# Optimization experiments

Hardware: AMD Instinct MI355X
Metric: run time of the kernel (lower is better)

Reference implementation:

```python
import jax, jax.numpy as jnp
import numpy as np

N_NODES = 50000
N_EDGES = 300000
N_GRAPHS = 2048
N_FEATS = 128
DIM_OUT = 32


def setup_inputs() -> dict:
    key = jax.random.key(0)
    ks = jax.random.split(key, 10)
    def glorot(k, shape):
        fan_in, fan_out = shape
        lim = (6.0 / (fan_in + fan_out)) ** 0.5
        return jax.random.uniform(k, shape, jnp.float32, -lim, lim)
    x = jax.random.normal(ks[0], (N_NODES, N_FEATS), jnp.float32)
    edge_index = jax.random.randint(ks[1], (2, N_EDGES), 0, N_NODES, jnp.int64)
    batch = jnp.sort(jax.random.randint(ks[2], (N_NODES,), 0, N_GRAPHS, jnp.int64))
    return {
        "x": x,
        "edge_index": edge_index,
        "batch": batch,
        "W1": glorot(ks[3], (N_FEATS, 256)), "b1": jnp.zeros((256,), jnp.float32),
        "W2": glorot(ks[4], (256, 256)),     "b2": jnp.zeros((256,), jnp.float32),
        "W3": glorot(ks[5], (256, 256)),     "b3": jnp.zeros((256,), jnp.float32),
        "Wf1": glorot(ks[6], (256, 128)),    "bf1": jnp.zeros((128,), jnp.float32),
        "Wf2": glorot(ks[7], (128, DIM_OUT)), "bf2": jnp.zeros((DIM_OUT,), jnp.float32),
    }


def _gcn_norm(edge_index, num_nodes):
    # PyG GCNConv default: add self-loops, symmetric D^-1/2 (A+I) D^-1/2 norm.
    loop = jnp.arange(num_nodes, dtype=edge_index.dtype)
    src = jnp.concatenate([edge_index[0], loop])
    dst = jnp.concatenate([edge_index[1], loop])
    deg = jax.ops.segment_sum(jnp.ones_like(dst, jnp.float32), dst, num_segments=num_nodes)
    dinv = jnp.where(deg > 0, deg ** -0.5, 0.0)
    norm = dinv[src] * dinv[dst]  # [E + N]
    return src, dst, norm


def _gcn_conv(x, src, dst, norm, W, b):
    h = x @ W                                # [N, C] transform first (efficient)
    msg = h[src] * norm[:, None]             # gather + scale, [E+N, C]
    agg = jax.ops.segment_sum(msg, dst, num_segments=x.shape[0])
    return agg + b


def reference(x, edge_index, batch, W1, b1, W2, b2, W3, b3, Wf1, bf1, Wf2, bf2):
    n = x.shape[0]
    src, dst, norm = _gcn_norm(edge_index, n)
    h = jax.nn.relu(_gcn_conv(x, src, dst, norm, W1, b1))
    h = jax.nn.relu(_gcn_conv(h, src, dst, norm, W2, b2))
    h = jax.nn.relu(_gcn_conv(h, src, dst, norm, W3, b3))
    # global_mean_pool over batch segment ids
    sums = jax.ops.segment_sum(h, batch, num_segments=N_GRAPHS)
    cnts = jax.ops.segment_sum(jnp.ones((n,), jnp.float32), batch, num_segments=N_GRAPHS)
    hg = sums / jnp.maximum(cnts, 1.0)[:, None]
    h = jax.nn.relu(hg @ Wf1 + bf1)
    return h @ Wf2 + bf2  # [N_GRAPHS, DIM_OUT]
```

## Files before the change

kernel.cpp:

```cpp
#include <hip/hip_runtime.h>
#include <hip/hip_bf16.h>

#define NNODES 50000
#define NEDGES 300000
#define NGRAPH 2048
#define NFEAT  128
#define NHID   256
#define DOUT   32
#define NROWS  50048

typedef __bf16 bf16x8 __attribute__((ext_vector_type(8)));
typedef float  f32x4  __attribute__((ext_vector_type(4)));
typedef unsigned short ushort8v __attribute__((ext_vector_type(8)));
typedef __attribute__((address_space(1))) const void* gas_ptr;
typedef __attribute__((address_space(3))) void* las_ptr;

__device__ __forceinline__ float bf2f(unsigned short u) {
    return __uint_as_float(((unsigned)u) << 16);
}
__device__ __forceinline__ unsigned short f2bf(float f) {
    unsigned u = __float_as_uint(f);
    unsigned r = u + 0x7FFFu + ((u >> 16) & 1u);
    return (unsigned short)(r >> 16);
}
__device__ __forceinline__ float sb2f(unsigned v, int k) {
    return (float)((signed char)(v >> (8 * k)));
}


__global__ __launch_bounds__(256) void prep_k(const float* __restrict__ x, unsigned short* __restrict__ x16,
                                              const float* __restrict__ W1, const float* __restrict__ W2,
                                              const float* __restrict__ W3, const float* __restrict__ Wf1,
                                              const float* __restrict__ Wf2,
                                              unsigned short* __restrict__ Wt1, unsigned short* __restrict__ Wt2,
                                              unsigned short* __restrict__ Wt3, unsigned short* __restrict__ Wf1t,
                                              unsigned short* __restrict__ Wf2t,
                                              int* __restrict__ cnt, int* __restrict__ fill,
                                              int4* __restrict__ adj8z, float4* __restrict__ hgz) {
    int idx = blockIdx.x * 256 + threadIdx.x;
    if (idx < 800000) {
        int i = idx * 8;
        float4 a = *(const float4*)&x[i];
        float4 b = *(const float4*)&x[i + 4];
        ushort8v o = { f2bf(a.x), f2bf(a.y), f2bf(a.z), f2bf(a.w),
                       f2bf(b.x), f2bf(b.y), f2bf(b.z), f2bf(b.w) };
        int row = idx >> 4, ch = idx & 15;
        ((ushort8v*)x16)[(size_t)(row << 4) | (ch ^ (row & 7))] = o;
        return;
    }
    int t = idx - 800000;
    if (t < 200704) {
        const float* W; unsigned short* Wt; int K, N, base; bool sw;
        if      (t <  32768) { W = W1;  Wt = Wt1;  K = 128; N = 256; base = 0;      sw = true; }
        else if (t <  98304) { W = W2;  Wt = Wt2;  K = 256; N = 256; base = 32768;  sw = true; }
        else if (t < 163840) { W = W3;  Wt = Wt3;  K = 256; N = 256; base = 98304;  sw = true; }
        else if (t < 196608) { W = Wf1; Wt = Wf1t; K = 256; N = 128; base = 163840; sw = false; }
        else                 { W = Wf2; Wt = Wf2t; K = 128; N = 32;  base = 196608; sw = false; }
        int i = t - base; int n = i / K, k = i - n * K;
        unsigned short v = f2bf(W[(size_t)k * N + n]);
        if (sw) Wt[(k >> 5) * 8192 + n * 32 + (k & 31)] = v;
        else    Wt[i] = v;
        return;
    }
    t -= 200704;
    if (t < NNODES) { cnt[t] = 0; fill[t] = 0; return; }
    t -= NNODES;
    if (t < 200000) { int4 z4 = {0, 0, 0, 0}; adj8z[t] = z4; return; }
    t -= 200000;
    if (t < 131072) { hgz[t] = make_float4(0.f, 0.f, 0.f, 0.f); }
}

__global__ __launch_bounds__(256) void edge_hist_k(const int* __restrict__ dst, int* cnt, int E) {
    int e = blockIdx.x * 256 + threadIdx.x;
    if (e < E) atomicAdd(&cnt[dst[e]], 1);
}

__global__ __launch_bounds__(1024) void scan_block_k(const int* __restrict__ cnt, int* __restrict__ rowp,
                                                     int* __restrict__ part, float* __restrict__ dinv,
                                                     int2* __restrict__ hdr, int n) {
    __shared__ int s[1024];
    int tid = threadIdx.x;
    int i = blockIdx.x * 1024 + tid;
    int v = (i < n) ? cnt[i] : 0;
    if (i < n) {
        float dv = rsqrtf((float)(v + 1));
        dinv[i] = dv;
        hdr[i] = make_int2(v, __float_as_int(dv * dv));
    }
    s[tid] = v;
    __syncthreads();
    for (int off = 1; off < 1024; off <<= 1) {
        int t = (tid >= off) ? s[tid - off] : 0;
        __syncthreads();
        s[tid] += t;
        __syncthreads();
    }
    if (i < n) rowp[i] = s[tid] - v;
    if (tid == 1023) part[blockIdx.x] = s[1023];
}

__global__ __launch_bounds__(256) void scatter_k(const int* __restrict__ src, const int* __restrict__ dst,
                                                 const int* __restrict__ rowp_pre, const int* __restrict__ part,
                                                 int* fill, const float* __restrict__ dinv,
                                                 int2* __restrict__ adj8, int2* __restrict__ adj,
                                                 int* __restrict__ rowp_fin,
                                                 const int* __restrict__ batch, int* __restrict__ gstart,
                                                 int E, int n, int nb) {
    __shared__ int s[64];
    int tid = threadIdx.x;
    if (tid < 64) s[tid] = (tid < nb) ? part[tid] : 0;
    __syncthreads();
    for (int off = 1; off < 64; off <<= 1) {
        int t = 0;
        if (tid < 64 && tid >= off) t = s[tid - off];
        __syncthreads();
        if (tid < 64) s[tid] += t;
        __syncthreads();
    }
    int gid = blockIdx.x * 256 + tid;
    if (gid <= n) {
        if (gid < n) {
            int ch = gid >> 10;
            int base = (ch == 0) ? 0 : s[ch - 1];
            rowp_fin[gid] = rowp_pre[gid] + base;
        } else {
            rowp_fin[n] = s[nb - 1];
        }
    }
    if (gid < n) {
        int b = batch[gid];
        int prev = (gid == 0) ? -1 : batch[gid - 1];
        for (int g = prev + 1; g <= b; ++g) gstart[g] = gid;
        if (gid == n - 1)
            for (int g = b + 1; g <= NGRAPH; ++g) gstart[g] = n;
    }
    if (gid < E) {
        int ss = src[gid], d = dst[gid];
        int f = atomicAdd(&fill[d], 1);
        int2 a; a.x = ss; a.y = __float_as_int(dinv[ss] * dinv[d]);
        if (f < 8) {
            adj8[d * 8 + f] = a;
        } else {
            int ch = d >> 10;
            int base = (ch == 0) ? 0 : s[ch - 1];
            adj[rowp_pre[d] + base + f] = a;
        }
    }
}

template<int CH>
__global__ __launch_bounds__(256) void agg_k(const unsigned short* __restrict__ T,
                                             const int4* __restrict__ adj8,
                                             const int2* __restrict__ hdr,
                                             const int* __restrict__ rowf,
                                             const int2* __restrict__ adj,
                                             unsigned short* __restrict__ z, int n) {
    int g  = threadIdx.x / CH;
    int li = threadIdx.x % CH;
    int node = blockIdx.x * (256 / CH) + g;
    if (node >= n) return;
    const ushort8v* tp = (const ushort8v*)T;
    int2 h = hdr[node];
    int deg = h.x;
    float sw = __int_as_float(h.y);
    ushort8v u = tp[(size_t)node * CH + (li ^ (node & 7))];
    int4 s4[4];
#pragma unroll
    for (int j = 0; j < 4; ++j) s4[j] = adj8[node * 4 + j];
    float ac[8];
#pragma unroll
    for (int k = 0; k < 8; ++k) ac[k] = bf2f(u[k]) * sw;
    int c[8]; float w[8];
#pragma unroll
    for (int j = 0; j < 4; ++j) {
        c[2 * j]     = s4[j].x; w[2 * j]     = __int_as_float(s4[j].y);
        c[2 * j + 1] = s4[j].z; w[2 * j + 1] = __int_as_float(s4[j].w);
    }
    ushort8v mm[8];
#pragma unroll
    for (int j = 0; j < 8; ++j) mm[j] = tp[(size_t)c[j] * CH + (li ^ (c[j] & 7))];
#pragma unroll
    for (int j = 0; j < 8; ++j)
#pragma unroll
        for (int k = 0; k < 8; ++k)
            ac[k] += bf2f(mm[j][k]) * w[j];
    if (deg > 8) {
        int e0 = rowf[node], e1 = e0 + deg;
        for (int e = e0 + 8; e < e1; e += 4) {
            int2 a2[4];
#pragma unroll
            for (int j = 0; j < 4; ++j) {
                int ee = e + j;
                a2[j] = (ee < e1) ? adj[ee] : make_int2(0, 0);
            }
            ushort8v m2[4];
#pragma unroll
            for (int j = 0; j < 4; ++j) m2[j] = tp[(size_t)a2[j].x * CH + (li ^ (a2[j].x & 7))];
#pragma unroll
            for (int j = 0; j < 4; ++j)
#pragma unroll
                for (int k = 0; k < 8; ++k)
                    ac[k] += bf2f(m2[j][k]) * __int_as_float(a2[j].y);
        }
    }
    ushort8v o;
#pragma unroll
    for (int k = 0; k < 8; ++k) o[k] = f2bf(ac[k]);
    ((ushort8v*)z)[(size_t)node * CH + (li ^ (node & 7))] = o;
}

__global__ __launch_bounds__(256) void agg_q_k(const unsigned char* __restrict__ Hq,
                                               const float* __restrict__ csc,
                                               const int4* __restrict__ adj8,
                                               const int2* __restrict__ hdr,
                                               const int* __restrict__ rowf,
                                               const int2* __restrict__ adj,
                                               unsigned short* __restrict__ z, int n) {
    int g  = threadIdx.x >> 4;
    int li = threadIdx.x & 15;
    int node = blockIdx.x * 16 + g;
    if (node >= n) return;
    const uint4* qp = (const uint4*)Hq;
    int2 h = hdr[node];
    int deg = h.x;
    float swgt = __int_as_float(h.y) * csc[node];
    uint4 u = qp[(size_t)node * 16 + li];
    int4 s4[4];
#pragma unroll
    for (int j = 0; j < 4; ++j) s4[j] = adj8[node * 4 + j];
    int c[8]; float w[8];
#pragma unroll
    for (int j = 0; j < 4; ++j) {
        c[2 * j]     = s4[j].x; w[2 * j]     = __int_as_float(s4[j].y);
        c[2 * j + 1] = s4[j].z; w[2 * j + 1] = __int_as_float(s4[j].w);
    }
    uint4 mm[8];
#pragma unroll
    for (int j = 0; j < 8; ++j) mm[j] = qp[(size_t)c[j] * 16 + li];
    float ws[8];
#pragma unroll
    for (int j = 0; j < 8; ++j) ws[j] = w[j] * csc[c[j]];
    float ac[16];
#pragma unroll
    for (int k = 0; k < 4; ++k) {
        ac[k]      = sb2f(u.x, k) * swgt;
        ac[k + 4]  = sb2f(u.y, k) * swgt;
        ac[k + 8]  = sb2f(u.z, k) * swgt;
        ac[k + 12] = sb2f(u.w, k) * swgt;
    }
#pragma unroll
    for (int j = 0; j < 8; ++j)
#pragma unroll
        for (int k = 0; k < 4; ++k) {
            ac[k]      += sb2f(mm[j].x, k) * ws[j];
            ac[k + 4]  += sb2f(mm[j].y, k) * ws[j];
            ac[k + 8]  += sb2f(mm[j].z, k) * ws[j];
            ac[k + 12] += sb2f(mm[j].w, k) * ws[j];
        }
    if (deg > 8) {
        int e0 = rowf[node], e1 = e0 + deg;
        for (int e = e0 + 8; e < e1; e += 4) {
            int2 a2[4];
#pragma unroll
            for (int j = 0; j < 4; ++j) {
                int ee = e + j;
                a2[j] = (ee < e1) ? adj[ee] : make_int2(0, 0);
            }
            uint4 m2[4]; float w2[4];
#pragma unroll
            for (int j = 0; j < 4; ++j) m2[j] = qp[(size_t)a2[j].x * 16 + li];
#pragma unroll
            for (int j = 0; j < 4; ++j) w2[j] = __int_as_float(a2[j].y) * csc[a2[j].x];
#pragma unroll
            for (int j = 0; j < 4; ++j)
#pragma unroll
                for (int k = 0; k < 4; ++k) {
                    ac[k]      += sb2f(m2[j].x, k) * w2[j];
                    ac[k + 4]  += sb2f(m2[j].y, k) * w2[j];
                    ac[k + 8]  += sb2f(m2[j].z, k) * w2[j];
                    ac[k + 12] += sb2f(m2[j].w, k) * w2[j];
                }
        }
    }
    ushort8v o0, o1;
#pragma unroll
    for (int k = 0; k < 8; ++k) { o0[k] = f2bf(ac[k]); o1[k] = f2bf(ac[k + 8]); }
    size_t base = (size_t)node * 32;
    ((ushort8v*)z)[base + ((2 * li)     ^ (node & 7))] = o0;
    ((ushort8v*)z)[base + ((2 * li + 1) ^ (node & 7))] = o1;
}

template<int K, int MODE>
__global__ __launch_bounds__(512, 2) void gemm_k(const unsigned short* __restrict__ A,
                                                 const unsigned short* __restrict__ Bsw,
                                                 const float* __restrict__ bias,
                                                 unsigned char* __restrict__ Cq,
                                                 float* __restrict__ csc,
                                                 float* __restrict__ HGacc,
                                                 const int* __restrict__ batch,
                                                 int M, int flags, int ntiles) {
    constexpr int CPR = K / 8;
    constexpr int LP  = (64 * CPR) / 512;
    __shared__ unsigned short At[64 * K];
    __shared__ unsigned short Et[64 * 264];
    __shared__ int sbatch[64];
    const int tid = threadIdx.x;
    const int lane = tid & 63;
    const int wave = tid >> 6;
    const int m = lane & 15, q = lane >> 4;
    const int wr = (wave >> 2) * 32;
    const int wc = (wave & 3) * 64;

    bf16x8 breg[K / 32][4];
#pragma unroll
    for (int kt = 0; kt < K / 32; ++kt)
#pragma unroll
        for (int j = 0; j < 4; ++j)
            breg[kt][j] = *(const bf16x8*)&Bsw[kt * 8192 + (wc + j * 16 + m) * 32 + q * 8];

    for (int t = blockIdx.x; t < ntiles; t += gridDim.x) {
        const size_t cbase = (size_t)t * 64 * CPR;
#pragma unroll
        for (int p = 0; p < LP; ++p) {
            int u = p * 512 + tid;
            __builtin_amdgcn_global_load_lds((gas_ptr)(A + (cbase + u) * 8),
                                             (las_ptr)&At[(p * 512 + wave * 64) * 8], 16, 0, 0);
        }
        __syncthreads();

        f32x4 acc[2][4] = {};
#pragma unroll
        for (int kt = 0; kt < K / 32; ++kt) {
            bf16x8 af[2];
#pragma unroll
            for (int i = 0; i < 2; ++i) {
                int lr = wr + i * 16 + m;
                af[i] = *(const bf16x8*)&At[(lr * CPR + ((kt * 4 + q) ^ (lr & 7))) * 8];
            }
#pragma unroll
            for (int i = 0; i < 2; ++i)
#pragma unroll
                for (int j = 0; j < 4; ++j)
                    acc[i][j] = __builtin_amdgcn_mfma_f32_16x16x32_bf16(af[i], breg[kt][j], acc[i][j], 0, 0, 0);
        }

#pragma unroll
        for (int i = 0; i < 2; ++i) {
#pragma unroll
            for (int j = 0; j < 4; ++j) {
                int c = wc + j * 16 + m;
                float bv = (flags & 2) ? bias[c] : 0.f;
#pragma unroll
                for (int r = 0; r < 4; ++r) {
                    float v = acc[i][j][r] + bv;
                    if (flags & 1) v = fmaxf(v, 0.f);
                    Et[(wr + i * 16 + q * 4 + r) * 264 + c] = f2bf(v);
                }
            }
        }
        if (MODE == 2 && tid < 64) {
            int rr = t * 64 + tid;
            sbatch[tid] = (rr < M) ? batch[rr] : -1;
        }
        __syncthreads();

        if (MODE == 1) {
            int row = tid >> 3, ch8 = tid & 7;
            int rr = t * 64 + row;
            ushort8v e[4];
#pragma unroll
            for (int k2 = 0; k2 < 4; ++k2)
                e[k2] = *(const ushort8v*)&Et[row * 264 + ch8 * 32 + k2 * 8];
            float mx = 0.f;
#pragma unroll
            for (int k2 = 0; k2 < 4; ++k2)
#pragma unroll
                for (int k = 0; k < 8; ++k) mx = fmaxf(mx, fabsf(bf2f(e[k2][k])));
            mx = fmaxf(mx, __shfl_xor(mx, 1, 64));
            mx = fmaxf(mx, __shfl_xor(mx, 2, 64));
            mx = fmaxf(mx, __shfl_xor(mx, 4, 64));
            float inv = (mx > 0.f) ? 127.f / mx : 0.f;
            unsigned pk[8];
#pragma unroll
            for (int w2 = 0; w2 < 8; ++w2) {
                unsigned p = 0;
#pragma unroll
                for (int b = 0; b < 4; ++b) {
                    int e8 = w2 * 4 + b;
                    float v = bf2f(e[e8 >> 3][e8 & 7]);
                    int qv = (int)rintf(v * inv);
                    p |= ((unsigned)(qv & 255)) << (8 * b);
                }
                pk[w2] = p;
            }
            if (rr < M) {
                uint4* dst = (uint4*)&Cq[(size_t)rr * 256 + ch8 * 32];
                dst[0] = make_uint4(pk[0], pk[1], pk[2], pk[3]);
                dst[1] = make_uint4(pk[4], pk[5], pk[6], pk[7]);
                if (ch8 == 0) csc[rr] = mx * (1.f / 127.f);
            }
        } else {
            int c = tid & 255, hh = tid >> 8;
            int gcur = sbatch[hh * 32];
            float acp = 0.f;
#pragma unroll 1
            for (int r = 0; r < 32; ++r) {
                int gb = sbatch[hh * 32 + r];
                if (gb != gcur) {
                    if (gcur >= 0) atomicAdd(&HGacc[(size_t)gcur * 256 + c], acp);
                    acp = 0.f; gcur = gb;
                }
                if (gb >= 0) acp += bf2f(Et[(hh * 32 + r) * 264 + c]);
            }
            if (gcur >= 0) atomicAdd(&HGacc[(size_t)gcur * 256 + c], acp);
        }
    }
}

__global__ __launch_bounds__(256) void mlp_head_k(const float* __restrict__ HGacc,
                                                  const int* __restrict__ gstart,
                                                  const unsigned short* __restrict__ Wf1t,
                                                  const unsigned short* __restrict__ Wf2t,
                                                  const float* __restrict__ bf1, const float* __restrict__ bf2,
                                                  float* __restrict__ out) {
    __shared__ unsigned short As1[128 * 32];
    __shared__ unsigned short Bs1[128 * 32];
    __shared__ unsigned short R[128 * 128];
    __shared__ unsigned short Bs2[32 * 128];
    __shared__ float invc[128];
    const int tid = threadIdx.x;
    const int lane = tid & 63, wave = tid >> 6;
    const int m = lane & 15, q = lane >> 4;
    const int rowBase = blockIdx.x * 128;
    const int wr = (wave >> 1) * 64;
    const int wc = (wave & 1) * 64;

#pragma unroll
    for (int c2 = 0; c2 < 2; ++c2) {
        const unsigned short* g = &Wf2t[(c2 * 256 + tid) * 8];
        __builtin_amdgcn_global_load_lds((gas_ptr)g, (las_ptr)&Bs2[(c2 * 256 + wave * 64) * 8], 16, 0, 0);
    }
    if (tid < 128) {
        int g0 = rowBase + tid;
        invc[tid] = 1.f / fmaxf((float)(gstart[g0 + 1] - gstart[g0]), 1.f);
    }
    __syncthreads();

    f32x4 acc[4][4] = {};
    for (int kt = 0; kt < 256; kt += 32) {
        {
            int row = tid >> 1, half = tid & 1;
            const float4* src = (const float4*)&HGacc[(size_t)(rowBase + row) * 256 + kt + half * 16];
            float4 f0 = src[0], f1 = src[1], f2 = src[2], f3 = src[3];
            float sc = invc[row];
            ushort8v p0 = { f2bf(f0.x * sc), f2bf(f0.y * sc), f2bf(f0.z * sc), f2bf(f0.w * sc),
                            f2bf(f1.x * sc), f2bf(f1.y * sc), f2bf(f1.z * sc), f2bf(f1.w * sc) };
            ushort8v p1 = { f2bf(f2.x * sc), f2bf(f2.y * sc), f2bf(f2.z * sc), f2bf(f2.w * sc),
                            f2bf(f3.x * sc), f2bf(f3.y * sc), f2bf(f3.z * sc), f2bf(f3.w * sc) };
            *(ushort8v*)&As1[row * 32 + half * 16] = p0;
            *(ushort8v*)&As1[row * 32 + half * 16 + 8] = p1;
        }
#pragma unroll
        for (int c2 = 0; c2 < 2; ++c2) {
            int u = c2 * 256 + tid;
            int row = u >> 2, kp = u & 3;
            const unsigned short* gb = &Wf1t[(size_t)row * 256 + kt + kp * 8];
            __builtin_amdgcn_global_load_lds((gas_ptr)gb, (las_ptr)&Bs1[(c2 * 256 + wave * 64) * 8], 16, 0, 0);
        }
        __syncthreads();
        bf16x8 af[4], bfr[4];
#pragma unroll
        for (int i = 0; i < 4; ++i) af[i] = *(const bf16x8*)&As1[(wr + i * 16 + m) * 32 + q * 8];
#pragma unroll
        for (int j = 0; j < 4; ++j) bfr[j] = *(const bf16x8*)&Bs1[(wc + j * 16 + m) * 32 + q * 8];
#pragma unroll
        for (int i = 0; i < 4; ++i)
#pragma unroll
            for (int j = 0; j < 4; ++j)
                acc[i][j] = __builtin_amdgcn_mfma_f32_16x16x32_bf16(af[i], bfr[j], acc[i][j], 0, 0, 0);
        __syncthreads();
    }
#pragma unroll
    for (int i = 0; i < 4; ++i)
#pragma unroll
        for (int j = 0; j < 4; ++j) {
            int c = wc + j * 16 + m;
            float bv = bf1[c];
#pragma unroll
            for (int r = 0; r < 4; ++r) {
                int rr = wr + i * 16 + q * 4 + r;
                R[rr * 128 + c] = f2bf(fmaxf(acc[i][j][r] + bv, 0.f));
            }
        }
    __syncthreads();

    const int wr2 = wave * 32;
    f32x4 acc2[2][2] = {};
#pragma unroll
    for (int s2 = 0; s2 < 4; ++s2) {
        bf16x8 af2[2], bf22[2];
#pragma unroll
        for (int i = 0; i < 2; ++i) af2[i] = *(const bf16x8*)&R[(wr2 + i * 16 + m) * 128 + s2 * 32 + q * 8];
#pragma unroll
        for (int ct = 0; ct < 2; ++ct) bf22[ct] = *(const bf16x8*)&Bs2[(ct * 16 + m) * 128 + s2 * 32 + q * 8];
#pragma unroll
        for (int i = 0; i < 2; ++i)
#pragma unroll
            for (int ct = 0; ct < 2; ++ct)
                acc2[i][ct] = __builtin_amdgcn_mfma_f32_16x16x32_bf16(af2[i], bf22[ct], acc2[i][ct], 0, 0, 0);
    }
#pragma unroll
    for (int i = 0; i < 2; ++i)
#pragma unroll
        for (int ct = 0; ct < 2; ++ct) {
            int c = ct * 16 + m;
            float bv = bf2[c];
#pragma unroll
            for (int r = 0; r < 4; ++r) {
                int rr = rowBase + wr2 + i * 16 + q * 4 + r;
                out[(size_t)rr * 32 + c] = acc2[i][ct][r] + bv;
            }
        }
}

extern "C" void kernel_launch(void* const* d_in, const int* in_sizes, int n_in,
                              void* d_out, int out_size, void* d_ws, size_t ws_size,
                              hipStream_t stream) {
    const float* x    = (const float*)d_in[0];
    const int*   ei   = (const int*)d_in[1];
    const int*   batch= (const int*)d_in[2];
    const float* W1   = (const float*)d_in[3];
    const float* b1   = (const float*)d_in[4];
    const float* W2   = (const float*)d_in[5];
    const float* b2   = (const float*)d_in[6];
    const float* W3   = (const float*)d_in[7];
    const float* b3   = (const float*)d_in[8];
    const float* Wf1  = (const float*)d_in[9];
    const float* bf1  = (const float*)d_in[10];
    const float* Wf2  = (const float*)d_in[11];
    const float* bf2  = (const float*)d_in[12];
    float* out = (float*)d_out;

    const int* e_src = ei;
    const int* e_dst = ei + NEDGES;

    char* ws = (char*)d_ws;
    size_t off = 0;
    auto alloc = [&](size_t bytes) -> void* {
        void* p = (void*)(ws + off);
        off += (bytes + 255) & ~(size_t)255;
        return p;
    };
    unsigned short* X16 = (unsigned short*)alloc((size_t)NROWS * NFEAT * 2);
    unsigned short* Za  = (unsigned short*)alloc((size_t)NROWS * NFEAT * 2);
    unsigned short* Zb  = (unsigned short*)alloc((size_t)NROWS * NHID * 2);
    unsigned char*  Hq  = (unsigned char*)alloc((size_t)NROWS * NHID);
    float*          csc = (float*)alloc((size_t)NROWS * 4);
    float*          HGacc = (float*)alloc((size_t)NGRAPH * NHID * 4);
    unsigned short* Wt1 = (unsigned short*)alloc((size_t)NHID * NFEAT * 2);
    unsigned short* Wt2 = (unsigned short*)alloc((size_t)NHID * NHID * 2);
    unsigned short* Wt3 = (unsigned short*)alloc((size_t)NHID * NHID * 2);
    unsigned short* Wf1t= (unsigned short*)alloc((size_t)NFEAT * NHID * 2);
    unsigned short* Wf2t= (unsigned short*)alloc((size_t)DOUT * NFEAT * 2);
    float* dinv = (float*)alloc((size_t)NNODES * 4);
    int*   cnt  = (int*)alloc((size_t)NNODES * 4);
    int*   fill = (int*)alloc((size_t)NNODES * 4);
    int*   rowp = (int*)alloc((size_t)(NNODES + 1) * 4);
    int*   rowf = (int*)alloc((size_t)(NNODES + 1) * 4);
    int2*  adj8 = (int2*)alloc((size_t)NNODES * 8 * 8);
    int2*  adj  = (int2*)alloc((size_t)NEDGES * 8);
    int2*  hdr  = (int2*)alloc((size_t)NNODES * 8);
    int*   part = (int*)alloc((size_t)64 * 4);
    int*   gstart = (int*)alloc((size_t)(NGRAPH + 1) * 4);
    (void)alloc(131072);

    const int nb = (NNODES + 1023) / 1024;

    hipLaunchKernelGGL(prep_k, dim3((1381776 + 255) / 256), dim3(256), 0, stream,
                       x, X16, W1, W2, W3, Wf1, Wf2, Wt1, Wt2, Wt3, Wf1t, Wf2t, cnt, fill,
                       (int4*)adj8, (float4*)HGacc);
    hipLaunchKernelGGL(edge_hist_k, dim3((NEDGES + 255) / 256), dim3(256), 0, stream, e_dst, cnt, NEDGES);
    hipLaunchKernelGGL(scan_block_k, dim3(nb), dim3(1024), 0, stream, cnt, rowp, part, dinv, hdr, NNODES);
    hipLaunchKernelGGL(scatter_k, dim3((NEDGES + 255) / 256), dim3(256), 0, stream,
                       e_src, e_dst, rowp, part, fill, dinv, adj8, adj, rowf, batch, gstart,
                       NEDGES, NNODES, nb);

    const int ntiles = NROWS / 64;
    hipLaunchKernelGGL((agg_k<16>), dim3((NNODES + 15) / 16), dim3(256), 0, stream,
                       X16, (const int4*)adj8, hdr, rowf, adj, Za, NNODES);
    hipLaunchKernelGGL((gemm_k<128, 1>), dim3(512), dim3(512), 0, stream,
                       Za, Wt1, b1, Hq, csc, (float*)nullptr, (const int*)nullptr, NNODES, 3, ntiles);
    hipLaunchKernelGGL(agg_q_k, dim3((NNODES + 15) / 16), dim3(256), 0, stream,
                       Hq, csc, (const int4*)adj8, hdr, rowf, adj, Zb, NNODES);
    hipLaunchKernelGGL((gemm_k<256, 1>), dim3(512), dim3(512), 0, stream,
                       Zb, Wt2, b2, Hq, csc, (float*)nullptr, (const int*)nullptr, NNODES, 3, ntiles);
    hipLaunchKernelGGL(agg_q_k, dim3((NNODES + 15) / 16), dim3(256), 0, stream,
                       Hq, csc, (const int4*)adj8, hdr, rowf, adj, Zb, NNODES);
    hipLaunchKernelGGL((gemm_k<256, 2>), dim3(512), dim3(512), 0, stream,
                       Zb, Wt3, b3, (unsigned char*)nullptr, (float*)nullptr, HGacc, batch, NNODES, 3, ntiles);

    hipLaunchKernelGGL(mlp_head_k, dim3(NGRAPH / 128), dim3(256), 0, stream,
                       HGacc, gstart, Wf1t, Wf2t, bf1, bf2, out);
}
```

Baseline: 275.6 us.

## Quantize input features to int8 and widen aggregation lanes per node

The input features are now quantized to int8 with a per-row scale in prep_k instead of converted to bf16, and a new agg_q1_k gathers these int8 rows for the first aggregation, halving the bytes gathered per neighbor. The layer 2/3 aggregation kernel is changed from 16 to 32 lanes per node with 8 bytes per lane, which halves the registers per thread and increases parallelism. The cost is lower precision on the raw inputs, plus an extra scale lookup per neighbor.

```diff
diff --git a/kernel.cpp b/kernel.cpp
--- a/kernel.cpp
+++ b/kernel.cpp
@@ -28,7 +28,8 @@
 }
 
 
-__global__ __launch_bounds__(256) void prep_k(const float* __restrict__ x, unsigned short* __restrict__ x16,
+__global__ __launch_bounds__(256) void prep_k(const float* __restrict__ x, unsigned char* __restrict__ Xq,
+                                              float* __restrict__ xsc,
                                               const float* __restrict__ W1, const float* __restrict__ W2,
                                               const float* __restrict__ W3, const float* __restrict__ Wf1,
                                               const float* __restrict__ Wf2,
@@ -39,13 +40,27 @@
                                               int4* __restrict__ adj8z, float4* __restrict__ hgz) {
     int idx = blockIdx.x * 256 + threadIdx.x;
     if (idx < 800000) {
-        int i = idx * 8;
-        float4 a = *(const float4*)&x[i];
-        float4 b = *(const float4*)&x[i + 4];
-        ushort8v o = { f2bf(a.x), f2bf(a.y), f2bf(a.z), f2bf(a.w),
-                       f2bf(b.x), f2bf(b.y), f2bf(b.z), f2bf(b.w) };
-        int row = idx >> 4, ch = idx & 15;
-        ((ushort8v*)x16)[(size_t)(row << 4) | (ch ^ (row & 7))] = o;
+        int row = idx >> 4, li = idx & 15;
+        const float4* xs = (const float4*)&x[(size_t)row * 128 + li * 8];
+        float4 a = xs[0], b = xs[1];
+        float m = fmaxf(fmaxf(fmaxf(fabsf(a.x), fabsf(a.y)), fmaxf(fabsf(a.z), fabsf(a.w))),
+                        fmaxf(fmaxf(fabsf(b.x), fabsf(b.y)), fmaxf(fabsf(b.z), fabsf(b.w))));
+        m = fmaxf(m, __shfl_xor(m, 1, 16));
+        m = fmaxf(m, __shfl_xor(m, 2, 16));
+        m = fmaxf(m, __shfl_xor(m, 4, 16));
+        m = fmaxf(m, __shfl_xor(m, 8, 16));
+        float inv = (m > 0.f) ? 127.f / m : 0.f;
+        float v[8] = {a.x, a.y, a.z, a.w, b.x, b.y, b.z, b.w};
+        unsigned w0 = 0, w1 = 0;
+#pragma unroll
+        for (int k = 0; k < 4; ++k) {
+            int q0 = (int)rintf(v[k] * inv);
+            int q1 = (int)rintf(v[k + 4] * inv);
+            w0 |= ((unsigned)(q0 & 255)) << (8 * k);
+            w1 |= ((unsigned)(q1 & 255)) << (8 * k);
+        }
+        ((uint2*)Xq)[(size_t)row * 16 + li] = make_uint2(w0, w1);
+        if (li == 0) xsc[row] = m * (1.f / 127.f);
         return;
     }
     int t = idx - 800000;
@@ -148,42 +163,50 @@
     }
 }
 
-template<int CH>
-__global__ __launch_bounds__(256) void agg_k(const unsigned short* __restrict__ T,
-                                             const int4* __restrict__ adj8,
-                                             const int2* __restrict__ hdr,
-                                             const int* __restrict__ rowf,
-                                             const int2* __restrict__ adj,
-                                             unsigned short* __restrict__ z, int n) {
-    int g  = threadIdx.x / CH;
-    int li = threadIdx.x % CH;
-    int node = blockIdx.x * (256 / CH) + g;
+__global__ __launch_bounds__(256) void agg_q1_k(const unsigned char* __restrict__ Xq,
+                                                const float* __restrict__ xsc,
+                                                const int4* __restrict__ adj8,
+                                                const int2* __restrict__ hdr,
+                                                const int* __restrict__ rowf,
+                                                const int2* __restrict__ adj,
+                                                unsigned short* __restrict__ z, int n) {
+    int g  = threadIdx.x >> 4;
+    int li = threadIdx.x & 15;
+    int node = blockIdx.x * 16 + g;
     if (node >= n) return;
-    const ushort8v* tp = (const ushort8v*)T;
+    const uint2* qp = (const uint2*)Xq;
     int2 h = hdr[node];
     int deg = h.x;
-    float sw = __int_as_float(h.y);
-    ushort8v u = tp[(size_t)node * CH + (li ^ (node & 7))];
+    float swgt = __int_as_float(h.y) * xsc[node];
+    uint2 u = qp[(size_t)node * 16 + li];
     int4 s4[4];
 #pragma unroll
     for (int j = 0; j < 4; ++j) s4[j] = adj8[node * 4 + j];
-    float ac[8];
-#pragma unroll
-    for (int k = 0; k < 8; ++k) ac[k] = bf2f(u[k]) * sw;
     int c[8]; float w[8];
 #pragma unroll
     for (int j = 0; j < 4; ++j) {
         c[2 * j]     = s4[j].x; w[2 * j]     = __int_as_float(s4[j].y);
         c[2 * j + 1] = s4[j].z; w[2 * j + 1] = __int_as_float(s4[j].w);
     }
-    ushort8v mm[8];
-#pragma unroll
-    for (int j = 0; j < 8; ++j) mm[j] = tp[(size_t)c[j] * CH + (li ^ (c[j] & 7))];
+    uint2 mm[8];
+#pragma unroll
+    for (int j = 0; j < 8; ++j) mm[j] = qp[(size_t)c[j] * 16 + li];
+    float ws[8];
+#pragma unroll
+    for (int j = 0; j < 8; ++j) ws[j] = w[j] * xsc[c[j]];
+    float ac[8];
+#pragma unroll
+    for (int k = 0; k < 4; ++k) {
+        ac[k]     = sb2f(u.x, k) * swgt;
+        ac[k + 4] = sb2f(u.y, k) * swgt;
+    }
 #pragma unroll
     for (int j = 0; j < 8; ++j)
 #pragma unroll
-        for (int k = 0; k < 8; ++k)
-            ac[k] += bf2f(mm[j][k]) * w[j];
+        for (int k = 0; k < 4; ++k) {
+            ac[k]     += sb2f(mm[j].x, k) * ws[j];
+            ac[k + 4] += sb2f(mm[j].y, k) * ws[j];
+        }
     if (deg > 8) {
         int e0 = rowf[node], e1 = e0 + deg;
         for (int e = e0 + 8; e < e1; e += 4) {
@@ -193,20 +216,24 @@
                 int ee = e + j;
                 a2[j] = (ee < e1) ? adj[ee] : make_int2(0, 0);
             }
-            ushort8v m2[4];
-#pragma unroll
-            for (int j = 0; j < 4; ++j) m2[j] = tp[(size_t)a2[j].x * CH + (li ^ (a2[j].x & 7))];
+            uint2 m2[4]; float w2[4];
+#pragma unroll
+            for (int j = 0; j < 4; ++j) m2[j] = qp[(size_t)a2[j].x * 16 + li];
+#pragma unroll
+            for (int j = 0; j < 4; ++j) w2[j] = __int_as_float(a2[j].y) * xsc[a2[j].x];
 #pragma unroll
             for (int j = 0; j < 4; ++j)
 #pragma unroll
-                for (int k = 0; k < 8; ++k)
-                    ac[k] += bf2f(m2[j][k]) * __int_as_float(a2[j].y);
+                for (int k = 0; k < 4; ++k) {
+                    ac[k]     += sb2f(m2[j].x, k) * w2[j];
+                    ac[k + 4] += sb2f(m2[j].y, k) * w2[j];
+                }
         }
     }
     ushort8v o;
 #pragma unroll
     for (int k = 0; k < 8; ++k) o[k] = f2bf(ac[k]);
-    ((ushort8v*)z)[(size_t)node * CH + (li ^ (node & 7))] = o;
+    ((ushort8v*)z)[(size_t)node * 16 + (li ^ (node & 7))] = o;
 }
 
 __global__ __launch_bounds__(256) void agg_q_k(const unsigned char* __restrict__ Hq,
@@ -216,15 +243,15 @@
                                                const int* __restrict__ rowf,
                                                const int2* __restrict__ adj,
                                                unsigned short* __restrict__ z, int n) {
-    int g  = threadIdx.x >> 4;
-    int li = threadIdx.x & 15;
-    int node = blockIdx.x * 16 + g;
+    int g  = threadIdx.x >> 5;
+    int li = threadIdx.x & 31;
+    int node = blockIdx.x * 8 + g;
     if (node >= n) return;
-    const uint4* qp = (const uint4*)Hq;
+    const uint2* qp = (const uint2*)Hq;
     int2 h = hdr[node];
     int deg = h.x;
     float swgt = __int_as_float(h.y) * csc[node];
-    uint4 u = qp[(size_t)node * 16 + li];
+    uint2 u = qp[(size_t)node * 32 + li];
     int4 s4[4];
 #pragma unroll
     for (int j = 0; j < 4; ++j) s4[j] = adj8[node * 4 + j];
@@ -234,28 +261,24 @@
         c[2 * j]     = s4[j].x; w[2 * j]     = __int_as_float(s4[j].y);
         c[2 * j + 1] = s4[j].z; w[2 * j + 1] = __int_as_float(s4[j].w);
     }
-    uint4 mm[8];
-#pragma unroll
-    for (int j = 0; j < 8; ++j) mm[j] = qp[(size_t)c[j] * 16 + li];
+    uint2 mm[8];
+#pragma unroll
+    for (int j = 0; j < 8; ++j) mm[j] = qp[(size_t)c[j] * 32 + li];
     float ws[8];
 #pragma unroll
     for (int j = 0; j < 8; ++j) ws[j] = w[j] * csc[c[j]];
-    float ac[16];
+    float ac[8];
 #pragma unroll
     for (int k = 0; k < 4; ++k) {
-        ac[k]      = sb2f(u.x, k) * swgt;
-        ac[k + 4]  = sb2f(u.y, k) * swgt;
-        ac[k + 8]  = sb2f(u.z, k) * swgt;
-        ac[k + 12] = sb2f(u.w, k) * swgt;
+        ac[k]     = sb2f(u.x, k) * swgt;
+        ac[k + 4] = sb2f(u.y, k) * swgt;
     }
 #pragma unroll
     for (int j = 0; j < 8; ++j)
 #pragma unroll
         for (int k = 0; k < 4; ++k) {
-            ac[k]      += sb2f(mm[j].x, k) * ws[j];
-            ac[k + 4]  += sb2f(mm[j].y, k) * ws[j];
-            ac[k + 8]  += sb2f(mm[j].z, k) * ws[j];
-            ac[k + 12] += sb2f(mm[j].w, k) * ws[j];
+            ac[k]     += sb2f(mm[j].x, k) * ws[j];
+            ac[k + 4] += sb2f(mm[j].y, k) * ws[j];
         }
     if (deg > 8) {
         int e0 = rowf[node], e1 = e0 + deg;
@@ -266,28 +289,24 @@
                 int ee = e + j;
                 a2[j] = (ee < e1) ? adj[ee] : make_int2(0, 0);
             }
-            uint4 m2[4]; float w2[4];
-#pragma unroll
-            for (int j = 0; j < 4; ++j) m2[j] = qp[(size_t)a2[j].x * 16 + li];
+            uint2 m2[4]; float w2[4];
+#pragma unroll
+            for (int j = 0; j < 4; ++j) m2[j] = qp[(size_t)a2[j].x * 32 + li];
 #pragma unroll
             for (int j = 0; j < 4; ++j) w2[j] = __int_as_float(a2[j].y) * csc[a2[j].x];
 #pragma unroll
             for (int j = 0; j < 4; ++j)
 #pragma unroll
                 for (int k = 0; k < 4; ++k) {
-                    ac[k]      += sb2f(m2[j].x, k) * w2[j];
-                    ac[k + 4]  += sb2f(m2[j].y, k) * w2[j];
-                    ac[k + 8]  += sb2f(m2[j].z, k) * w2[j];
-                    ac[k + 12] += sb2f(m2[j].w, k) * w2[j];
+                    ac[k]     += sb2f(m2[j].x, k) * w2[j];
+                    ac[k + 4] += sb2f(m2[j].y, k) * w2[j];
                 }
         }
     }
-    ushort8v o0, o1;
-#pragma unroll
-    for (int k = 0; k < 8; ++k) { o0[k] = f2bf(ac[k]); o1[k] = f2bf(ac[k + 8]); }
-    size_t base = (size_t)node * 32;
-    ((ushort8v*)z)[base + ((2 * li)     ^ (node & 7))] = o0;
-    ((ushort8v*)z)[base + ((2 * li + 1) ^ (node & 7))] = o1;
+    ushort8v o;
+#pragma unroll
+    for (int k = 0; k < 8; ++k) o[k] = f2bf(ac[k]);
+    ((ushort8v*)z)[(size_t)node * 32 + (li ^ (node & 7))] = o;
 }
 
 template<int K, int MODE>
@@ -551,7 +570,8 @@
         off += (bytes + 255) & ~(size_t)255;
         return p;
     };
-    unsigned short* X16 = (unsigned short*)alloc((size_t)NROWS * NFEAT * 2);
+    unsigned char*  Xq  = (unsigned char*)alloc((size_t)NROWS * NFEAT);
+    float*          xsc = (float*)alloc((size_t)NROWS * 4);
     unsigned short* Za  = (unsigned short*)alloc((size_t)NROWS * NFEAT * 2);
     unsigned short* Zb  = (unsigned short*)alloc((size_t)NROWS * NHID * 2);
     unsigned char*  Hq  = (unsigned char*)alloc((size_t)NROWS * NHID);
@@ -577,7 +597,7 @@
     const int nb = (NNODES + 1023) / 1024;
 
     hipLaunchKernelGGL(prep_k, dim3((1381776 + 255) / 256), dim3(256), 0, stream,
-                       x, X16, W1, W2, W3, Wf1, Wf2, Wt1, Wt2, Wt3, Wf1t, Wf2t, cnt, fill,
+                       x, Xq, xsc, W1, W2, W3, Wf1, Wf2, Wt1, Wt2, Wt3, Wf1t, Wf2t, cnt, fill,
                        (int4*)adj8, (float4*)HGacc);
     hipLaunchKernelGGL(edge_hist_k, dim3((NEDGES + 255) / 256), dim3(256), 0, stream, e_dst, cnt, NEDGES);
     hipLaunchKernelGGL(scan_block_k, dim3(nb), dim3(1024), 0, stream, cnt, rowp, part, dinv, hdr, NNODES);
@@ -586,15 +606,15 @@
                        NEDGES, NNODES, nb);
 
     const int ntiles = NROWS / 64;
-    hipLaunchKernelGGL((agg_k<16>), dim3((NNODES + 15) / 16), dim3(256), 0, stream,
-                       X16, (const int4*)adj8, hdr, rowf, adj, Za, NNODES);
+    hipLaunchKernelGGL(agg_q1_k, dim3((NNODES + 15) / 16), dim3(256), 0, stream,
+                       Xq, xsc, (const int4*)adj8, hdr, rowf, adj, Za, NNODES);
     hipLaunchKernelGGL((gemm_k<128, 1>), dim3(512), dim3(512), 0, stream,
                        Za, Wt1, b1, Hq, csc, (float*)nullptr, (const int*)nullptr, NNODES, 3, ntiles);
-    hipLaunchKernelGGL(agg_q_k, dim3((NNODES + 15) / 16), dim3(256), 0, stream,
+    hipLaunchKernelGGL(agg_q_k, dim3((NNODES + 7) / 8), dim3(256), 0, stream,
                        Hq, csc, (const int4*)adj8, hdr, rowf, adj, Zb, NNODES);
     hipLaunchKernelGGL((gemm_k<256, 1>), dim3(512), dim3(512), 0, stream,
                        Zb, Wt2, b2, Hq, csc, (float*)nullptr, (const int*)nullptr, NNODES, 3, ntiles);
-    hipLaunchKernelGGL(agg_q_k, dim3((NNODES + 15) / 16), dim3(256), 0, stream,
+    hipLaunchKernelGGL(agg_q_k, dim3((NNODES + 7) / 8), dim3(256), 0, stream,
                        Hq, csc, (const int4*)adj8, hdr, rowf, adj, Zb, NNODES);
     hipLaunchKernelGGL((gemm_k<256, 2>), dim3(512), dim3(512), 0, stream,
                        Zb, Wt3, b3, (unsigned char*)nullptr, (float*)nullptr, HGacc, batch, NNODES, 3, ntiles);
```

Result: no change. 274.9 us (-0.3%).
